# Kernel tuning notes

Measured on AMD Instinct MI355X. Metric: run time of the kernel, lower is better.

## Reference

```python
import jax, jax.numpy as jnp
import numpy as np

N, L, S, D, HD, FC = 4, 2048, 2048, 256, 256, 8  # batch, query len, source len, in_depth, hidden_depth, heads
EPS = 1e-12  # F.normalize eps


def setup_inputs() -> dict:
    key = jax.random.key(0)
    ks = jax.random.split(key, 8)
    sc = 0.05
    return {
        "x0": jax.random.normal(ks[0], (N, L, D), jnp.float32),
        "x1": jax.random.normal(ks[1], (N, S, D), jnp.float32),
        "W0": jax.random.normal(ks[2], (D, HD), jnp.float32) * sc,
        "b0": jax.random.normal(ks[3], (HD,), jnp.float32) * sc,
        "W1": jax.random.normal(ks[4], (D, 2 * HD), jnp.float32) * sc,
        "b1": jax.random.normal(ks[5], (2 * HD,), jnp.float32) * sc,
        "Wm": jax.random.normal(ks[6], (HD, D), jnp.float32) * sc,
        "bm": jax.random.normal(ks[7], (D,), jnp.float32) * sc,
        "alpha": jnp.ones((1,), jnp.float32),
        "beta": jnp.zeros((1,), jnp.float32),
    }


def _l2norm(x):
    # F.normalize(dim=2): x / max(||x||, eps)
    return x / jnp.maximum(jnp.linalg.norm(x, axis=2, keepdims=True), EPS)


def reference(x0, x1, W0, b0, W1, b1, Wm, bm, alpha, beta):
    n, l, _ = x0.shape
    s = x1.shape[1]
    fc = FC
    m = n * fc
    # projections + head split: 'n l (fc c) -> (n fc) l c'
    x0p = (x0 @ W0 + b0).reshape(n, l, fc, -1).transpose(0, 2, 1, 3).reshape(m, l, -1)
    x1p = (x1 @ W1 + b1).reshape(n, s, fc, -1).transpose(0, 2, 1, 3).reshape(m, s, -1)
    x1_point, x1_value = jnp.split(x1p, 2, axis=2)  # each (m, s, c)
    # cosine similarity (m, l, s)
    sim = jnp.einsum('mlc,msc->mls', _l2norm(x0p), _l2norm(x1_point))
    sim = jax.nn.sigmoid(alpha * sim + beta)
    max_val = jnp.max(sim, axis=2)              # (m, l)
    max_idx = jnp.argmax(sim, axis=2)           # (m, l)
    gathered = jnp.take_along_axis(x1_value, max_idx[:, :, None], axis=1)  # (m, l, c)
    new_x0 = max_val[:, :, None] * gathered
    # '(n fc) l c -> n l (fc c)'
    new_x0 = new_x0.reshape(n, fc, l, -1).transpose(0, 2, 1, 3).reshape(n, l, -1)
    return new_x0 @ Wm + bm
```

## Files before the change

kernel.cpp:

```cpp
#include <hip/hip_runtime.h>
#include <hip/hip_bf16.h>
#include <cmath>

#define NB   4
#define LQ   2048
#define SK   2048
#define DD   256
#define HD   256
#define FC   8
#define CH   32
#define MHEAD 32

#define MARGIN 0.0085f
#define CAP    16

typedef float f32x16 __attribute__((ext_vector_type(16)));
typedef float f32x2  __attribute__((ext_vector_type(2)));
typedef short bf16x8 __attribute__((ext_vector_type(8)));
typedef unsigned short ushort8v __attribute__((ext_vector_type(8)));

__device__ inline unsigned short f32_to_bf16_bits(float v) {
    __hip_bfloat16 b = __float2bfloat16(v);
    return __builtin_bit_cast(unsigned short, b);
}
__device__ inline unsigned int ord_encode(float v) {
    unsigned int u = __float_as_uint(v);
    return (u & 0x80000000u) ? ~u : (u | 0x80000000u);
}
__device__ inline float ord_decode(unsigned int e) {
    unsigned int u = (e & 0x80000000u) ? (e & 0x7fffffffu) : ~e;
    return __uint_as_float(u);
}

#define MFMA32(a, b, c) __builtin_amdgcn_mfma_f32_32x32x16_bf16(a, b, c, 0, 0, 0)

__global__ __launch_bounds__(256, 7)
void proj_gemm_kernel(const float* __restrict__ x0, const float* __restrict__ x1,
                      const float* __restrict__ W0, const float* __restrict__ b0f,
                      const float* __restrict__ W1, const float* __restrict__ b1f,
                      float* __restrict__ xq, float* __restrict__ xk)
{
    __shared__ float As[2][16][68];
    __shared__ float Bs[2][16][64];
    const int nt  = blockIdx.x;
    const bool is0 = (nt < 4);
    const float* A    = is0 ? x0 : x1;
    const float* B    = is0 ? W0 : W1;
    const float* bias = is0 ? b0f : b1f;
    float* dst        = is0 ? xq : xk;
    const int NB_ = is0 ? HD : 2 * HD;
    const int hw  = is0 ? 32 : 64;
    const int bm  = blockIdx.y * 64;
    const int K   = DD;

    const int tx = threadIdx.x & 15;
    const int ty = threadIdx.x >> 4;
    f32x2 acc2[4][2] = {};

    const int arow = threadIdx.x >> 2;
    const int akq  = (threadIdx.x & 3) << 2;
    const int bkr  = threadIdx.x >> 4;
    const int bnq  = (threadIdx.x & 15) << 2;
    const int fl   = (nt & 3) * 2 + (bnq >> 5);
    const int bcol = fl * hw + (bnq & 31);

    {
        const float4 a4 = *(const float4*)&A[(size_t)(bm + arow) * K + akq];
        const float4 b4 = *(const float4*)&B[(size_t)bkr * NB_ + bcol];
        As[0][akq + 0][arow] = a4.x;
        As[0][akq + 1][arow] = a4.y;
        As[0][akq + 2][arow] = a4.z;
        As[0][akq + 3][arow] = a4.w;
        *(float4*)&Bs[0][bkr][bnq] = b4;
    }
    __syncthreads();

    const int nchunk = K >> 4;
    float4 pa, pb;
    for (int c = 0; c < nchunk; ++c) {
        const int cur = c & 1;
        if (c + 1 < nchunk) {
            const int k0 = (c + 1) << 4;
            pa = *(const float4*)&A[(size_t)(bm + arow) * K + k0 + akq];
            pb = *(const float4*)&B[(size_t)(k0 + bkr) * NB_ + bcol];
        }
        #pragma unroll
        for (int kk = 0; kk < 16; ++kk) {
            const float4 a4 = *(const float4*)&As[cur][kk][ty << 2];
            const f32x2 b01 = *(const f32x2*)&Bs[cur][kk][tx << 2];
            const f32x2 b23 = *(const f32x2*)&Bs[cur][kk][(tx << 2) + 2];
            const float av[4] = {a4.x, a4.y, a4.z, a4.w};
            #pragma unroll
            for (int i = 0; i < 4; ++i) {
                const f32x2 aa = {av[i], av[i]};
                acc2[i][0] = __builtin_elementwise_fma(aa, b01, acc2[i][0]);
                acc2[i][1] = __builtin_elementwise_fma(aa, b23, acc2[i][1]);
            }
        }
        if (c + 1 < nchunk) {
            const int nxt = cur ^ 1;
            As[nxt][akq + 0][arow] = pa.x;
            As[nxt][akq + 1][arow] = pa.y;
            As[nxt][akq + 2][arow] = pa.z;
            As[nxt][akq + 3][arow] = pa.w;
            *(float4*)&Bs[nxt][bkr][bnq] = pb;
        }
        __syncthreads();
    }

    #pragma unroll
    for (int i = 0; i < 4; ++i) {
        const int row = bm + (ty << 2) + i;
        const int n = row >> 11, l = row & 2047;
        #pragma unroll
        for (int j = 0; j < 4; ++j) {
            const int cl = (tx << 2) + j;
            const int f  = (nt & 3) * 2 + (cl >> 5);
            const int cc = cl & 31;
            const float v = acc2[i][j >> 1][j & 1] + bias[f * hw + cc];
            dst[((((size_t)n * FC + f) * LQ) + l) * CH + cc] = v;
        }
    }
}

__global__ __launch_bounds__(256)
void prep_kernel(const float* __restrict__ x1, const float* __restrict__ Wm,
                 const float* __restrict__ W1,
                 unsigned short* __restrict__ x1b,
                 unsigned short* __restrict__ wm_s,
                 unsigned short* __restrict__ wv_s)
{
    const int i = blockIdx.x * 256 + threadIdx.x;
    if (i < 262144) {
        const float4 a = *(const float4*)(x1 + (size_t)i * 8);
        const float4 b = *(const float4*)(x1 + (size_t)i * 8 + 4);
        ushort8v o;
        o[0] = f32_to_bf16_bits(a.x); o[1] = f32_to_bf16_bits(a.y);
        o[2] = f32_to_bf16_bits(a.z); o[3] = f32_to_bf16_bits(a.w);
        o[4] = f32_to_bf16_bits(b.x); o[5] = f32_to_bf16_bits(b.y);
        o[6] = f32_to_bf16_bits(b.z); o[7] = f32_to_bf16_bits(b.w);
        *(ushort8v*)(x1b + (size_t)i * 8) = o;
    } else if (i < 262144 + 65536) {
        const int j = i - 262144;
        const int k = j >> 8, n = j & 255;
        wm_s[(k >> 4) * 4096 + n * 16 + (k & 15)] = f32_to_bf16_bits(Wm[k * 256 + n]);
    } else {
        const int j = i - 327680;
        const int k = j >> 8, v = j & 255;
        const int w = (v >> 5) * 64 + 32 + (v & 31);
        wv_s[(k >> 4) * 4096 + v * 16 + (k & 15)] = f32_to_bf16_bits(W1[k * 512 + w]);
    }
}

__global__ __launch_bounds__(256)
void val_gemm_kernel(const unsigned short* __restrict__ x1b,
                     const unsigned short* __restrict__ wv_s,
                     const float* __restrict__ b1f, float* __restrict__ xv)
{
    const int wave = threadIdx.x >> 6;
    const int lane = threadIdx.x & 63;
    const int idx  = blockIdx.x * 4 + wave;
    const int mt   = idx >> 3;
    const int nt   = idx & 7;
    const int col  = lane & 31;
    const int g8   = (lane >> 5) * 8;

    const unsigned short* aptr = x1b + (size_t)(mt * 32 + col) * 256 + g8;
    const unsigned short* bptr = wv_s + nt * 32 * 16 + col * 16 + g8;

    f32x16 acc = {0.f, 0.f, 0.f, 0.f, 0.f, 0.f, 0.f, 0.f,
                  0.f, 0.f, 0.f, 0.f, 0.f, 0.f, 0.f, 0.f};
    #pragma unroll 4
    for (int kc = 0; kc < 16; ++kc) {
        const bf16x8 a = *(const bf16x8*)(aptr + kc * 16);
        const bf16x8 bfr = *(const bf16x8*)(bptr + (size_t)kc * 4096);
        acc = MFMA32(a, bfr, acc);
    }

    const int v = nt * 32 + col;
    const int f = v >> 5, c = v & 31;
    const float bias = b1f[f * 64 + 32 + c];
    #pragma unroll
    for (int r = 0; r < 16; ++r) {
        const int g = mt * 32 + (r & 3) + 8 * (r >> 2) + 4 * (lane >> 5);
        const int n = g >> 11, s = g & 2047;
        xv[((((size_t)n * FC + f) * SK) + s) * CH + c] = acc[r] + bias;
    }
}

__global__ __launch_bounds__(256)
void norm_split_init_kernel(float* __restrict__ xq, unsigned short* __restrict__ qhi,
                            float* __restrict__ xk, unsigned short* __restrict__ khi,
                            const float* __restrict__ alpha,
                            unsigned int* __restrict__ maxhh_u, int* __restrict__ cnt)
{
    int r = blockIdx.x * blockDim.x + threadIdx.x;
    float* p;
    unsigned short* dhi;
    float sgn = 1.f;
    if (r < MHEAD * LQ) {
        maxhh_u[r] = 0u;
        cnt[r] = 0;
        p   = xq + (size_t)r * CH;
        dhi = qhi + (size_t)r * CH;
        if (alpha[0] < 0.f) sgn = -1.f;
    } else {
        r -= MHEAD * LQ;
        p   = xk + (size_t)r * CH;
        dhi = khi + (size_t)r * CH;
    }

    float4 v[8];
    float ss = 0.f;
    #pragma unroll
    for (int i = 0; i < 8; ++i) {
        v[i] = *(const float4*)(p + i * 4);
        ss = fmaf(v[i].x, v[i].x, ss);
        ss = fmaf(v[i].y, v[i].y, ss);
        ss = fmaf(v[i].z, v[i].z, ss);
        ss = fmaf(v[i].w, v[i].w, ss);
    }
    const float inv = sgn / fmaxf(sqrtf(ss), 1e-12f);

    ushort8v hb[4];
    #pragma unroll
    for (int i = 0; i < 8; ++i) {
        float4 w;
        w.x = v[i].x * inv; w.y = v[i].y * inv;
        w.z = v[i].z * inv; w.w = v[i].w * inv;
        *(float4*)(p + i * 4) = w;
        hb[i >> 1][(i & 1) * 4 + 0] = f32_to_bf16_bits(w.x);
        hb[i >> 1][(i & 1) * 4 + 1] = f32_to_bf16_bits(w.y);
        hb[i >> 1][(i & 1) * 4 + 2] = f32_to_bf16_bits(w.z);
        hb[i >> 1][(i & 1) * 4 + 3] = f32_to_bf16_bits(w.w);
    }
    #pragma unroll
    for (int i = 0; i < 4; ++i)
        *(ushort8v*)(dhi + i * 8) = hb[i];
}

__global__ __launch_bounds__(256, 4)
void maxpass_kernel(const unsigned short* __restrict__ qhi,
                    const unsigned short* __restrict__ khi,
                    unsigned int* __restrict__ maxhh_u)
{
    const int b    = blockIdx.x;
    const int sc   = b & 3;
    const int qb   = (b >> 2) & 15;
    const int h    = b >> 6;
    const int wave = threadIdx.x >> 6;
    const int lane = threadIdx.x & 63;
    const int qbase = qb * 128 + wave * 32;
    const int col   = lane & 31;
    const int g8    = (lane >> 5) * 8;

    const size_t qoff = ((size_t)h * LQ + qbase + col) * CH + g8;
    const bf16x8 ah0 = *(const bf16x8*)(qhi + qoff);
    const bf16x8 ah1 = *(const bf16x8*)(qhi + qoff + 16);

    const unsigned short* kh = khi + ((size_t)h * SK + sc * 512) * CH;
    const size_t koff = (size_t)col * CH + g8;

    float maxv[16];
    #pragma unroll
    for (int r = 0; r < 16; ++r) maxv[r] = -INFINITY;

    bf16x8 t0a = *(const bf16x8*)(kh + koff);
    bf16x8 t0b = *(const bf16x8*)(kh + koff + 16);
    bf16x8 t1a = *(const bf16x8*)(kh + koff + 32 * CH);
    bf16x8 t1b = *(const bf16x8*)(kh + koff + 32 * CH + 16);

    for (int sb = 0; sb < 16; sb += 2) {
        const bf16x8 c0a = t0a, c0b = t0b, c1a = t1a, c1b = t1b;
        if (sb + 2 < 16) {
            const size_t o = koff + (size_t)(sb + 2) * 32 * CH;
            t0a = *(const bf16x8*)(kh + o);
            t0b = *(const bf16x8*)(kh + o + 16);
            t1a = *(const bf16x8*)(kh + o + 32 * CH);
            t1b = *(const bf16x8*)(kh + o + 32 * CH + 16);
        }
        f32x16 c = {0.f, 0.f, 0.f, 0.f, 0.f, 0.f, 0.f, 0.f,
                    0.f, 0.f, 0.f, 0.f, 0.f, 0.f, 0.f, 0.f};
        c = MFMA32(ah0, c0a, c);
        c = MFMA32(ah1, c0b, c);
        f32x16 d = {0.f, 0.f, 0.f, 0.f, 0.f, 0.f, 0.f, 0.f,
                    0.f, 0.f, 0.f, 0.f, 0.f, 0.f, 0.f, 0.f};
        d = MFMA32(ah0, c1a, d);
        d = MFMA32(ah1, c1b, d);
        #pragma unroll
        for (int r = 0; r < 16; ++r)
            maxv[r] = fmaxf(maxv[r], fmaxf(c[r], d[r]));
    }

    #pragma unroll
    for (int r = 0; r < 16; ++r) {
        float v = maxv[r];
        #pragma unroll
        for (int m = 16; m >= 1; m >>= 1)
            v = fmaxf(v, __shfl_xor(v, m, 64));
        maxv[r] = v;
    }
    if (col == 0) {
        const int rbase = h * LQ + qbase + 4 * (lane >> 5);
        #pragma unroll
        for (int r = 0; r < 16; ++r)
            atomicMax(&maxhh_u[rbase + (r & 3) + 8 * (r >> 2)], ord_encode(maxv[r]));
    }
}

__global__ __launch_bounds__(256, 4)
void candpass_kernel(const unsigned short* __restrict__ qhi,
                     const unsigned short* __restrict__ khi,
                     const unsigned int* __restrict__ maxhh_u,
                     int* __restrict__ cnt, int* __restrict__ cand)
{
    const int b    = blockIdx.x;
    const int sc   = b & 3;
    const int qb   = (b >> 2) & 15;
    const int h    = b >> 6;
    const int wave = threadIdx.x >> 6;
    const int lane = threadIdx.x & 63;
    const int qbase = qb * 128 + wave * 32;
    const int col   = lane & 31;
    const int g8    = (lane >> 5) * 8;

    const size_t qoff = ((size_t)h * LQ + qbase + col) * CH + g8;
    const bf16x8 ah0 = *(const bf16x8*)(qhi + qoff);
    const bf16x8 ah1 = *(const bf16x8*)(qhi + qoff + 16);

    int   rows[16];
    float thr[16];
    {
        const int rbase = h * LQ + qbase + 4 * (lane >> 5);
        #pragma unroll
        for (int r = 0; r < 16; ++r) {
            rows[r] = rbase + (r & 3) + 8 * (r >> 2);
            thr[r]  = ord_decode(maxhh_u[rows[r]]) - MARGIN;
        }
    }

    const unsigned short* kh = khi + ((size_t)h * SK + sc * 512) * CH;
    const size_t koff = (size_t)col * CH + g8;
    const int sbase = sc * 512;

    bf16x8 t0a = *(const bf16x8*)(kh + koff);
    bf16x8 t0b = *(const bf16x8*)(kh + koff + 16);
    bf16x8 t1a = *(const bf16x8*)(kh + koff + 32 * CH);
    bf16x8 t1b = *(const bf16x8*)(kh + koff + 32 * CH + 16);

    for (int sb = 0; sb < 16; sb += 2) {
        const bf16x8 c0a = t0a, c0b = t0b, c1a = t1a, c1b = t1b;
        if (sb + 2 < 16) {
            const size_t o = koff + (size_t)(sb + 2) * 32 * CH;
            t0a = *(const bf16x8*)(kh + o);
            t0b = *(const bf16x8*)(kh + o + 16);
            t1a = *(const bf16x8*)(kh + o + 32 * CH);
            t1b = *(const bf16x8*)(kh + o + 32 * CH + 16);
        }
        f32x16 c = {0.f, 0.f, 0.f, 0.f, 0.f, 0.f, 0.f, 0.f,
                    0.f, 0.f, 0.f, 0.f, 0.f, 0.f, 0.f, 0.f};
        c = MFMA32(ah0, c0a, c);
        c = MFMA32(ah1, c0b, c);
        f32x16 d = {0.f, 0.f, 0.f, 0.f, 0.f, 0.f, 0.f, 0.f,
                    0.f, 0.f, 0.f, 0.f, 0.f, 0.f, 0.f, 0.f};
        d = MFMA32(ah0, c1a, d);
        d = MFMA32(ah1, c1b, d);

        unsigned int hit = 0u;
        #pragma unroll
        for (int r = 0; r < 16; ++r) {
            const float e = fmaxf(c[r], d[r]);
            hit = (e >= thr[r]) ? (hit | (1u << r)) : hit;
        }
        if (hit) {
            const int s0 = sbase + sb * 32 + col;
            #pragma unroll
            for (int r = 0; r < 16; ++r) {
                if (hit & (1u << r)) {
                    if (c[r] >= thr[r]) {
                        const int slot = atomicAdd(&cnt[rows[r]], 1);
                        if (slot < CAP) cand[(size_t)rows[r] * CAP + slot] = s0;
                    }
                    if (d[r] >= thr[r]) {
                        const int slot = atomicAdd(&cnt[rows[r]], 1);
                        if (slot < CAP) cand[(size_t)rows[r] * CAP + slot] = s0 + 32;
                    }
                }
            }
        }
    }
}

__global__ __launch_bounds__(256)
void refine_gather_kernel(const float* __restrict__ qn,
                          const float* __restrict__ kn,
                          const int* __restrict__ cnt, const int* __restrict__ cand,
                          const float* __restrict__ xv,
                          const float* __restrict__ alpha, const float* __restrict__ beta,
                          unsigned short* __restrict__ nxb)
{
    const int r = blockIdx.x * blockDim.x + threadIdx.x;
    const int h = r >> 11, l = r & 2047;

    float qr[CH];
    #pragma unroll
    for (int i = 0; i < 8; ++i) {
        const float4 v = *(const float4*)(qn + (size_t)r * CH + i * 4);
        qr[i * 4 + 0] = v.x; qr[i * 4 + 1] = v.y;
        qr[i * 4 + 2] = v.z; qr[i * 4 + 3] = v.w;
    }

    int m = cnt[r];
    if (m > CAP) m = CAP;
    float best = -INFINITY;
    int   bidx = 0x7fffffff;
    for (int j = 0; j < m; ++j) {
        const int s = cand[(size_t)r * CAP + j];
        const float4* k4 = (const float4*)(kn + ((size_t)h * SK + s) * CH);
        float p = 0.f;
        #pragma unroll
        for (int c = 0; c < 8; ++c) {
            const float4 kv = k4[c];
            p = fmaf(qr[c * 4 + 0], kv.x, p);
            p = fmaf(qr[c * 4 + 1], kv.y, p);
            p = fmaf(qr[c * 4 + 2], kv.z, p);
            p = fmaf(qr[c * 4 + 3], kv.w, p);
        }
        if (p > best || (p == best && s < bidx)) { best = p; bidx = s; }
    }
    if (bidx == 0x7fffffff) bidx = 0;

    const float a = alpha[0], be = beta[0];
    float tv;
    int idx = bidx;
    if (a == 0.f) { idx = 0; tv = be; }
    else          { tv = fmaf(fabsf(a), best, be); }
    float val;
    if (tv >= 0.f) val = 1.f / (1.f + expf(-tv));
    else           { const float e = expf(tv); val = e / (1.f + e); }

    const float4* vr = (const float4*)(xv + ((size_t)h * SK + idx) * CH);
    const int n = h >> 3, f = h & 7;
    unsigned short* out = nxb + (((size_t)n * LQ + l) * (FC * CH)) + f * CH;
    #pragma unroll
    for (int i = 0; i < 8; ++i) {
        const float4 w = vr[i];
        ushort8v o;
        o[0] = f32_to_bf16_bits(w.x * val);
        o[1] = f32_to_bf16_bits(w.y * val);
        o[2] = f32_to_bf16_bits(w.z * val);
        o[3] = f32_to_bf16_bits(w.w * val);
        *(unsigned long long*)(out + i * 4) = __builtin_bit_cast(unsigned long long,
            *(const ulong1*)&o);
    }
}

__global__ __launch_bounds__(256)
void gemm_out_mfma_kernel(const unsigned short* __restrict__ nxb,
                          const unsigned short* __restrict__ wm_s,
                          const float* __restrict__ bm, float* __restrict__ out)
{
    const int wave = threadIdx.x >> 6;
    const int lane = threadIdx.x & 63;
    const int idx  = blockIdx.x * 4 + wave;
    const int mt   = idx >> 3;
    const int nt   = idx & 7;
    const int col  = lane & 31;
    const int g8   = (lane >> 5) * 8;

    const unsigned short* aptr = nxb + (size_t)(mt * 32 + col) * 256 + g8;
    const unsigned short* bptr = wm_s + nt * 32 * 16 + col * 16 + g8;

    f32x16 acc = {0.f, 0.f, 0.f, 0.f, 0.f, 0.f, 0.f, 0.f,
                  0.f, 0.f, 0.f, 0.f, 0.f, 0.f, 0.f, 0.f};
    #pragma unroll 4
    for (int kc = 0; kc < 16; ++kc) {
        const bf16x8 a = *(const bf16x8*)(aptr + kc * 16);
        const bf16x8 bfr = *(const bf16x8*)(bptr + (size_t)kc * 4096);
        acc = MFMA32(a, bfr, acc);
    }

    const int n0 = nt * 32;
    const float bias = bm[n0 + col];
    #pragma unroll
    for (int r = 0; r < 16; ++r) {
        const int row = mt * 32 + (r & 3) + 8 * (r >> 2) + 4 * (lane >> 5);
        out[(size_t)row * 256 + n0 + col] = acc[r] + bias;
    }
}

extern "C" void kernel_launch(void* const* d_in, const int* in_sizes, int n_in,
                              void* d_out, int out_size, void* d_ws, size_t ws_size,
                              hipStream_t stream)
{
    const float* x0 = (const float*)d_in[0];
    const float* x1 = (const float*)d_in[1];
    const float* W0 = (const float*)d_in[2];
    const float* b0 = (const float*)d_in[3];
    const float* W1 = (const float*)d_in[4];
    const float* b1 = (const float*)d_in[5];
    const float* Wm = (const float*)d_in[6];
    const float* bm = (const float*)d_in[7];
    const float* alpha = (const float*)d_in[8];
    const float* beta  = (const float*)d_in[9];
    float* out = (float*)d_out;

    char* ws = (char*)d_ws;
    const size_t MB = 1024ull * 1024ull;
    float* x0q = (float*)(ws + 0);
    float* x1k = (float*)(ws + 8 * MB);
    float* x1v = (float*)(ws + 16 * MB);
    unsigned short* qhi = (unsigned short*)(ws + 24 * MB);
    unsigned short* khi = (unsigned short*)(ws + 28 * MB);
    unsigned short* x1b = (unsigned short*)(ws + 32 * MB);
    int* cand = (int*)(ws + 32 * MB);
    unsigned int* maxhh_u = (unsigned int*)(ws + 36 * MB);
    int* cnt  = (int*)(ws + 36 * MB + 256 * 1024);
    unsigned short* wm_s = (unsigned short*)(ws + 36 * MB + 512 * 1024);
    unsigned short* wv_s = (unsigned short*)(ws + 36 * MB + 640 * 1024);
    unsigned short* nxb  = (unsigned short*)(ws + 24 * MB);

    const int Mrows = NB * LQ;

    proj_gemm_kernel<<<dim3(8, Mrows / 64), 256, 0, stream>>>(
        x0, x1, W0, b0, W1, b1, x0q, x1k);
    prep_kernel<<<1536, 256, 0, stream>>>(x1, Wm, W1, x1b, wm_s, wv_s);
    val_gemm_kernel<<<512, 256, 0, stream>>>(x1b, wv_s, b1, x1v);
    norm_split_init_kernel<<<(2 * MHEAD * LQ) / 256, 256, 0, stream>>>(
        x0q, qhi, x1k, khi, alpha, maxhh_u, cnt);
    maxpass_kernel<<<2048, 256, 0, stream>>>(qhi, khi, maxhh_u);
    candpass_kernel<<<2048, 256, 0, stream>>>(qhi, khi, maxhh_u, cnt, cand);
    refine_gather_kernel<<<(MHEAD * LQ) / 256, 256, 0, stream>>>(
        x0q, x1k, cnt, cand, x1v, alpha, beta, nxb);
    gemm_out_mfma_kernel<<<512, 256, 0, stream>>>(nxb, wm_s, bm, out);
}
```

Measured before the change: 139.6 us.

## Stage K tiles through double-buffered padded LDS in max and candidate passes

The max pass and the candidate pass now load each 128-row key tile into a double-buffered shared-memory buffer once per block, instead of every wave reading keys straight from global memory. Rows are padded to 40 elements to avoid bank conflicts, and the next tile is prefetched while MFMAs run on the current one. This removes four-fold redundant global key loads across waves, at the cost of LDS traffic and block-wide barriers. Separately, the fp32 GEMM inner loop replaces two f32x2 LDS reads with a single float4 read.

```diff
diff --git a/kernel.cpp b/kernel.cpp
--- a/kernel.cpp
+++ b/kernel.cpp
@@ -13,6 +13,8 @@
 
 #define MARGIN 0.0085f
 #define CAP    16
+
+#define KROW 40
 
 typedef float f32x16 __attribute__((ext_vector_type(16)));
 typedef float f32x2  __attribute__((ext_vector_type(2)));
@@ -87,8 +89,9 @@
         #pragma unroll
         for (int kk = 0; kk < 16; ++kk) {
             const float4 a4 = *(const float4*)&As[cur][kk][ty << 2];
-            const f32x2 b01 = *(const f32x2*)&Bs[cur][kk][tx << 2];
-            const f32x2 b23 = *(const f32x2*)&Bs[cur][kk][(tx << 2) + 2];
+            const float4 bv = *(const float4*)&Bs[cur][kk][tx << 2];
+            const f32x2 b01 = {bv.x, bv.y};
+            const f32x2 b23 = {bv.z, bv.w};
             const float av[4] = {a4.x, a4.y, a4.z, a4.w};
             #pragma unroll
             for (int i = 0; i < 4; ++i) {
@@ -244,12 +247,14 @@
                     const unsigned short* __restrict__ khi,
                     unsigned int* __restrict__ maxhh_u)
 {
+    __shared__ unsigned short kbuf[2][128 * KROW];
     const int b    = blockIdx.x;
     const int sc   = b & 3;
     const int qb   = (b >> 2) & 15;
     const int h    = b >> 6;
     const int wave = threadIdx.x >> 6;
     const int lane = threadIdx.x & 63;
+    const int t    = threadIdx.x;
     const int qbase = qb * 128 + wave * 32;
     const int col   = lane & 31;
     const int g8    = (lane >> 5) * 8;
@@ -259,37 +264,46 @@
     const bf16x8 ah1 = *(const bf16x8*)(qhi + qoff + 16);
 
     const unsigned short* kh = khi + ((size_t)h * SK + sc * 512) * CH;
-    const size_t koff = (size_t)col * CH + g8;
+
+    const int srow  = t >> 1;
+    const int shalf = (t & 1) * 16;
+    const unsigned short* sp = kh + (size_t)srow * CH + shalf;
 
     float maxv[16];
     #pragma unroll
     for (int r = 0; r < 16; ++r) maxv[r] = -INFINITY;
 
-    bf16x8 t0a = *(const bf16x8*)(kh + koff);
-    bf16x8 t0b = *(const bf16x8*)(kh + koff + 16);
-    bf16x8 t1a = *(const bf16x8*)(kh + koff + 32 * CH);
-    bf16x8 t1b = *(const bf16x8*)(kh + koff + 32 * CH + 16);
-
-    for (int sb = 0; sb < 16; sb += 2) {
-        const bf16x8 c0a = t0a, c0b = t0b, c1a = t1a, c1b = t1b;
-        if (sb + 2 < 16) {
-            const size_t o = koff + (size_t)(sb + 2) * 32 * CH;
-            t0a = *(const bf16x8*)(kh + o);
-            t0b = *(const bf16x8*)(kh + o + 16);
-            t1a = *(const bf16x8*)(kh + o + 32 * CH);
-            t1b = *(const bf16x8*)(kh + o + 32 * CH + 16);
-        }
-        f32x16 c = {0.f, 0.f, 0.f, 0.f, 0.f, 0.f, 0.f, 0.f,
-                    0.f, 0.f, 0.f, 0.f, 0.f, 0.f, 0.f, 0.f};
-        c = MFMA32(ah0, c0a, c);
-        c = MFMA32(ah1, c0b, c);
-        f32x16 d = {0.f, 0.f, 0.f, 0.f, 0.f, 0.f, 0.f, 0.f,
-                    0.f, 0.f, 0.f, 0.f, 0.f, 0.f, 0.f, 0.f};
-        d = MFMA32(ah0, c1a, d);
-        d = MFMA32(ah1, c1b, d);
-        #pragma unroll
-        for (int r = 0; r < 16; ++r)
-            maxv[r] = fmaxf(maxv[r], fmaxf(c[r], d[r]));
+    bf16x8 s0 = *(const bf16x8*)(sp);
+    bf16x8 s1 = *(const bf16x8*)(sp + 8);
+    *(bf16x8*)(&kbuf[0][srow * KROW + shalf])     = s0;
+    *(bf16x8*)(&kbuf[0][srow * KROW + shalf + 8]) = s1;
+    __syncthreads();
+
+    for (int g = 0; g < 4; ++g) {
+        if (g < 3) {
+            const unsigned short* spn = sp + (size_t)(g + 1) * 128 * CH;
+            s0 = *(const bf16x8*)(spn);
+            s1 = *(const bf16x8*)(spn + 8);
+        }
+        const unsigned short* kbp = &kbuf[g & 1][0];
+        #pragma unroll
+        for (int tt = 0; tt < 4; ++tt) {
+            const int rl = tt * 32 + col;
+            const bf16x8 ka  = *(const bf16x8*)(kbp + rl * KROW + g8);
+            const bf16x8 kbv = *(const bf16x8*)(kbp + rl * KROW + 16 + g8);
+            f32x16 c = {0.f, 0.f, 0.f, 0.f, 0.f, 0.f, 0.f, 0.f,
+                        0.f, 0.f, 0.f, 0.f, 0.f, 0.f, 0.f, 0.f};
+            c = MFMA32(ah0, ka, c);
+            c = MFMA32(ah1, kbv, c);
+            #pragma unroll
+            for (int r = 0; r < 16; ++r) maxv[r] = fmaxf(maxv[r], c[r]);
+        }
+        if (g < 3) {
+            unsigned short* swn = &kbuf[(g + 1) & 1][srow * KROW + shalf];
+            *(bf16x8*)(swn)     = s0;
+            *(bf16x8*)(swn + 8) = s1;
+            __syncthreads();
+        }
     }
 
     #pragma unroll
@@ -314,12 +328,14 @@
                      const unsigned int* __restrict__ maxhh_u,
                      int* __restrict__ cnt, int* __restrict__ cand)
 {
+    __shared__ unsigned short kbuf[2][128 * KROW];
     const int b    = blockIdx.x;
     const int sc   = b & 3;
     const int qb   = (b >> 2) & 15;
     const int h    = b >> 6;
     const int wave = threadIdx.x >> 6;
     const int lane = threadIdx.x & 63;
+    const int t    = threadIdx.x;
     const int qbase = qb * 128 + wave * 32;
     const int col   = lane & 31;
     const int g8    = (lane >> 5) * 8;
@@ -340,53 +356,55 @@
     }
 
     const unsigned short* kh = khi + ((size_t)h * SK + sc * 512) * CH;
-    const size_t koff = (size_t)col * CH + g8;
     const int sbase = sc * 512;
 
-    bf16x8 t0a = *(const bf16x8*)(kh + koff);
-    bf16x8 t0b = *(const bf16x8*)(kh + koff + 16);
-    bf16x8 t1a = *(const bf16x8*)(kh + koff + 32 * CH);
-    bf16x8 t1b = *(const bf16x8*)(kh + koff + 32 * CH + 16);
-
-    for (int sb = 0; sb < 16; sb += 2) {
-        const bf16x8 c0a = t0a, c0b = t0b, c1a = t1a, c1b = t1b;
-        if (sb + 2 < 16) {
-            const size_t o = koff + (size_t)(sb + 2) * 32 * CH;
-            t0a = *(const bf16x8*)(kh + o);
-            t0b = *(const bf16x8*)(kh + o + 16);
-            t1a = *(const bf16x8*)(kh + o + 32 * CH);
-            t1b = *(const bf16x8*)(kh + o + 32 * CH + 16);
-        }
-        f32x16 c = {0.f, 0.f, 0.f, 0.f, 0.f, 0.f, 0.f, 0.f,
-                    0.f, 0.f, 0.f, 0.f, 0.f, 0.f, 0.f, 0.f};
-        c = MFMA32(ah0, c0a, c);
-        c = MFMA32(ah1, c0b, c);
-        f32x16 d = {0.f, 0.f, 0.f, 0.f, 0.f, 0.f, 0.f, 0.f,
-                    0.f, 0.f, 0.f, 0.f, 0.f, 0.f, 0.f, 0.f};
-        d = MFMA32(ah0, c1a, d);
-        d = MFMA32(ah1, c1b, d);
-
-        unsigned int hit = 0u;
-        #pragma unroll
-        for (int r = 0; r < 16; ++r) {
-            const float e = fmaxf(c[r], d[r]);
-            hit = (e >= thr[r]) ? (hit | (1u << r)) : hit;
-        }
-        if (hit) {
-            const int s0 = sbase + sb * 32 + col;
+    const int srow  = t >> 1;
+    const int shalf = (t & 1) * 16;
+    const unsigned short* sp = kh + (size_t)srow * CH + shalf;
+
+    bf16x8 s0 = *(const bf16x8*)(sp);
+    bf16x8 s1 = *(const bf16x8*)(sp + 8);
+    *(bf16x8*)(&kbuf[0][srow * KROW + shalf])     = s0;
+    *(bf16x8*)(&kbuf[0][srow * KROW + shalf + 8]) = s1;
+    __syncthreads();
+
+    for (int g = 0; g < 4; ++g) {
+        if (g < 3) {
+            const unsigned short* spn = sp + (size_t)(g + 1) * 128 * CH;
+            s0 = *(const bf16x8*)(spn);
+            s1 = *(const bf16x8*)(spn + 8);
+        }
+        const unsigned short* kbp = &kbuf[g & 1][0];
+        #pragma unroll
+        for (int tt = 0; tt < 4; ++tt) {
+            const int rl = tt * 32 + col;
+            const bf16x8 ka  = *(const bf16x8*)(kbp + rl * KROW + g8);
+            const bf16x8 kbv = *(const bf16x8*)(kbp + rl * KROW + 16 + g8);
+            f32x16 c = {0.f, 0.f, 0.f, 0.f, 0.f, 0.f, 0.f, 0.f,
+                        0.f, 0.f, 0.f, 0.f, 0.f, 0.f, 0.f, 0.f};
+            c = MFMA32(ah0, ka, c);
+            c = MFMA32(ah1, kbv, c);
+
+            unsigned int hit = 0u;
             #pragma unroll
-            for (int r = 0; r < 16; ++r) {
-                if (hit & (1u << r)) {
-                    if (c[r] >= thr[r]) {
+            for (int r = 0; r < 16; ++r)
+                hit = (c[r] >= thr[r]) ? (hit | (1u << r)) : hit;
+            if (hit) {
+                const int s = sbase + g * 128 + tt * 32 + col;
+                #pragma unroll
+                for (int r = 0; r < 16; ++r) {
+                    if (hit & (1u << r)) {
                         const int slot = atomicAdd(&cnt[rows[r]], 1);
-                        if (slot < CAP) cand[(size_t)rows[r] * CAP + slot] = s0;
-                    }
-                    if (d[r] >= thr[r]) {
-                        const int slot = atomicAdd(&cnt[rows[r]], 1);
-                        if (slot < CAP) cand[(size_t)rows[r] * CAP + slot] = s0 + 32;
+                        if (slot < CAP) cand[(size_t)rows[r] * CAP + slot] = s;
                     }
                 }
             }
+        }
+        if (g < 3) {
+            unsigned short* swn = &kbuf[(g + 1) & 1][srow * KROW + shalf];
+            *(bf16x8*)(swn)     = s0;
+            *(bf16x8*)(swn + 8) = s1;
+            __syncthreads();
         }
     }
 }
```

New measurement: 134.8 us. -3.4%, faster.
